# Performance work log

Measured on AMD Instinct MI355X. Metric: run time of the kernel, lower is better.

Reference implementation:

```python
import jax, jax.numpy as jnp
import numpy as np

D_MODEL = 1024


def bitlinear(x, weight):
    # ternary quantization with straight-through estimator; forward value is w_q*scale
    scale = jnp.clip(jnp.mean(jnp.abs(weight), axis=1, keepdims=True), 1e-5, None)
    w_q = jnp.clip(jnp.round(weight / scale), -1.0, 1.0)
    w = weight + jax.lax.stop_gradient(w_q * scale - weight)
    return x @ w.T


def rmsnorm(x, w, eps=1e-6):
    return x * jax.lax.rsqrt(jnp.mean(x * x, axis=-1, keepdims=True) + eps) * w


def setup_inputs() -> dict:
    key = jax.random.key(0)
    ks = jax.random.split(key, 6)
    D = D_MODEL
    std = np.sqrt(2.0 / D)  # kaiming_normal fan_out
    return {
        "x": jax.random.normal(ks[0], (4, 4096, D), dtype=jnp.float32),
        "Wr": jax.random.normal(ks[1], (D, D), dtype=jnp.float32) * std,
        "Wk": jax.random.normal(ks[2], (D, D), dtype=jnp.float32) * std,
        "Wv": jax.random.normal(ks[3], (D, D), dtype=jnp.float32) * std,
        "Wo": jax.random.normal(ks[4], (D, D), dtype=jnp.float32) * std,
        "decay": jnp.ones((D,), dtype=jnp.float32) * 0.99,
        "ln_w": jnp.ones((D,), dtype=jnp.float32),
    }


def reference(x, Wr, Wk, Wv, Wo, decay, ln_w):
    B, T, D = x.shape
    r = jax.nn.sigmoid(bitlinear(x, Wr))
    k = bitlinear(x, Wk)
    v = bitlinear(x, Wv)
    dec = jax.nn.sigmoid(decay)                              # [D]
    kv = k * v                                               # [B,T,D]
    positions = jnp.arange(T, dtype=x.dtype)                 # [T]
    log_decay = jnp.log(jnp.clip(dec, 1e-7, None))           # [D]
    scale = jnp.exp(positions[:, None] * log_decay[None, :])  # [T,D]
    scaled = kv / jnp.clip(scale, 1e-10, None)[None]         # [B,T,D]
    cum = jnp.cumsum(scaled, axis=1)                         # [B,T,D]
    state = cum * scale[None]                                # [B,T,D]
    return bitlinear(rmsnorm(r * state, ln_w), Wo)
```

## Files before the change

### kernel.cpp

```cpp
#include <hip/hip_runtime.h>

typedef unsigned short u16;
typedef __attribute__((ext_vector_type(8))) short bf16x8;
typedef __attribute__((ext_vector_type(4))) float f32x4;
typedef __attribute__((ext_vector_type(4))) unsigned short u16x4;

#define DM 1024

__device__ __forceinline__ float bf2f(u16 u){
  union { unsigned int i; float f; } v; v.i = ((unsigned int)u)<<16; return v.f;
}
__device__ __forceinline__ u16 f2bf(float f){
  unsigned int x = __float_as_uint(f);
  return (u16)((x + 0x7FFFu + ((x>>16)&1u)) >> 16);
}

__global__ __launch_bounds__(256)
void quantize_w(const float* __restrict__ W0, const float* __restrict__ W1,
                const float* __restrict__ W2, const float* __restrict__ W3,
                u16* __restrict__ wq, float* __restrict__ wsc)
{
  const int gr   = blockIdx.x*4 + (threadIdx.x>>6);
  const int lane = threadIdx.x & 63;
  const float* W; int row;
  if (gr < 1024)      { W = W0; row = gr; }
  else if (gr < 3072) { row = (gr-1024)>>1; W = (gr&1) ? W2 : W1; }
  else                { W = W3; row = gr-3072; }
  const float* wr = W + (size_t)row*DM;
  float4 v[4]; float s = 0.f;
  #pragma unroll
  for (int c=0;c<4;c++){
    v[c] = *(const float4*)&wr[c*256 + lane*4];
    s += fabsf(v[c].x)+fabsf(v[c].y)+fabsf(v[c].z)+fabsf(v[c].w);
  }
  #pragma unroll
  for (int off=32; off; off>>=1) s += __shfl_down(s, off);
  s = __shfl(s, 0);
  const float scale = fmaxf(s*(1.f/1024.f), 1e-5f);
  if (lane==0) wsc[gr] = scale;
  u16* wo = wq + (size_t)gr*DM;
  #pragma unroll
  for (int c=0;c<4;c++){
    u16x4 q;
    q[0] = f2bf(fminf(fmaxf(rintf(v[c].x/scale),-1.f),1.f));
    q[1] = f2bf(fminf(fmaxf(rintf(v[c].y/scale),-1.f),1.f));
    q[2] = f2bf(fminf(fmaxf(rintf(v[c].z/scale),-1.f),1.f));
    q[3] = f2bf(fminf(fmaxf(rintf(v[c].w/scale),-1.f),1.f));
    *(u16x4*)&wo[c*256 + lane*4] = q;
  }
}

__global__ void cvt_x(const float* __restrict__ x, u16* __restrict__ xb){
  const int i = (blockIdx.x*256 + threadIdx.x)*4;
  float4 v = *(const float4*)&x[i];
  u16x4 o; o[0]=f2bf(v.x); o[1]=f2bf(v.y); o[2]=f2bf(v.z); o[3]=f2bf(v.w);
  *(u16x4*)&xb[i] = o;
}


#define SB0 __builtin_amdgcn_sched_barrier(0)
#define WL4  do{ asm volatile("s_waitcnt lgkmcnt(4)" ::: "memory"); SB0; }while(0)
#define WL12 do{ asm volatile("s_waitcnt lgkmcnt(12)" ::: "memory"); SB0; }while(0)
#define WL0  do{ asm volatile("s_waitcnt lgkmcnt(0)" ::: "memory"); SB0; }while(0)
#define VM4  do{ asm volatile("s_waitcnt vmcnt(4)" ::: "memory"); SB0; }while(0)
#define VM0  do{ asm volatile("s_waitcnt vmcnt(0)" ::: "memory"); SB0; }while(0)
#define BARR do{ SB0; __builtin_amdgcn_s_barrier(); SB0; }while(0)

#define STG(gB, off, T, Q, buf) \
  __builtin_amdgcn_global_load_lds( \
    (const __attribute__((address_space(1))) void*)((const char*)(gB) + (off) + (Q)*131072 + (size_t)(T)*128), \
    (__attribute__((address_space(3))) void*)((char*)(buf) + ldst + (Q)*8192), 16, 0, 0)

#define RD(base, off) (*(const bf16x8*)((const char*)(base) + (off)))

#define MFMA16(AF, B, MI) \
  __builtin_amdgcn_s_setprio(1); \
  _Pragma("unroll") \
  for (int ni=0; ni<4; ++ni){ \
    acc[MI][ni]   = __builtin_amdgcn_mfma_f32_16x16x32_bf16(AF[0], B[ni],   acc[MI][ni],   0,0,0); \
    acc[MI][ni]   = __builtin_amdgcn_mfma_f32_16x16x32_bf16(AF[1], B[4+ni], acc[MI][ni],   0,0,0); \
    acc[MI+1][ni] = __builtin_amdgcn_mfma_f32_16x16x32_bf16(AF[2], B[ni],   acc[MI+1][ni], 0,0,0); \
    acc[MI+1][ni] = __builtin_amdgcn_mfma_f32_16x16x32_bf16(AF[3], B[4+ni], acc[MI+1][ni], 0,0,0); \
  } \
  __builtin_amdgcn_s_setprio(0)

#define TILE(T, C, BCUR, BNXT) { \
  const char* la  = (const char*)sA[C]; \
  const char* lnA = (const char*)sA[(C)^1]; \
  const char* lnB = (const char*)sB[(C)^1]; \
   \
  ay[0]=RD(la, arow+2*2048+koff0); ay[1]=RD(la, arow+2*2048+koff1); \
  ay[2]=RD(la, arow+3*2048+koff0); ay[3]=RD(la, arow+3*2048+koff1); \
  if ((T)+1<nt){ STG(Ag, aoff, (T)+1, 0, sA[(C)^1]); STG(Ag, aoff, (T)+1, 1, sA[(C)^1]); \
                 STG(Ag, aoff, (T)+1, 2, sA[(C)^1]); STG(Ag, aoff, (T)+1, 3, sA[(C)^1]); } \
  WL4; MFMA16(ax, BCUR, 0); BARR; \
   \
  ax[0]=RD(la, arow+4*2048+koff0); ax[1]=RD(la, arow+4*2048+koff1); \
  ax[2]=RD(la, arow+5*2048+koff0); ax[3]=RD(la, arow+5*2048+koff1); \
  if ((T)+2<nt){ STG(Bg, boff, (T)+2, 0, sB[C]); STG(Bg, boff, (T)+2, 1, sB[C]); } \
  WL4; MFMA16(ay, BCUR, 2); BARR; \
   \
  ay[0]=RD(la, arow+6*2048+koff0); ay[1]=RD(la, arow+6*2048+koff1); \
  ay[2]=RD(la, arow+7*2048+koff0); ay[3]=RD(la, arow+7*2048+koff1); \
  if ((T)+2<nt){ STG(Bg, boff, (T)+2, 2, sB[C]); STG(Bg, boff, (T)+2, 3, sB[C]); } \
  WL4; MFMA16(ax, BCUR, 4); SB0; \
  if ((T)==nt-2) { VM0; } else if ((T)<nt-2) { VM4; } \
  BARR; \
   \
  if ((T)<nt-1){ \
    BNXT[0]=RD(lnB, brow+0*2048+koff0); BNXT[1]=RD(lnB, brow+1*2048+koff0); \
    BNXT[2]=RD(lnB, brow+2*2048+koff0); BNXT[3]=RD(lnB, brow+3*2048+koff0); \
    BNXT[4]=RD(lnB, brow+0*2048+koff1); BNXT[5]=RD(lnB, brow+1*2048+koff1); \
    BNXT[6]=RD(lnB, brow+2*2048+koff1); BNXT[7]=RD(lnB, brow+3*2048+koff1); \
    ax[0]=RD(lnA, arow+0*2048+koff0); ax[1]=RD(lnA, arow+0*2048+koff1); \
    ax[2]=RD(lnA, arow+1*2048+koff0); ax[3]=RD(lnA, arow+1*2048+koff1); \
    WL12; \
  } else { WL0; } \
  MFMA16(ay, BCUR, 6); BARR; \
}

template<int MODE>
__global__ __launch_bounds__(512, 2)
void gemm_p(const u16* __restrict__ Ag, const u16* __restrict__ Bg,
            const float* __restrict__ bscale,
            u16* __restrict__ o_r, u16* __restrict__ o_kv,
            float* __restrict__ o_f)
{
  __shared__ u16 sA[2][256*64];
  __shared__ u16 sB[2][256*64];
  const int tid = threadIdx.x, wave = tid>>6, lane = tid&63;
  const int lr = lane&15, lg = lane>>4;
  const int wm = wave>>2, wn = wave&3;
  const int bm0 = blockIdx.x*256, bn0 = blockIdx.y*256;
  constexpr int nt = 16;

  const int r8   = lane>>3;
  const int scol = ((lane&7)<<4) ^ (r8<<4);
  const size_t aoff = (size_t)(bm0 + wave*8 + r8)*2048 + scol;
  const size_t boff = (size_t)(bn0 + wave*8 + r8)*2048 + scol;
  const int ldst = wave*1024;
  const int S = (lr&7)<<4;
  const int koff0 = (0  + (lg<<4)) ^ S;
  const int koff1 = (64 + (lg<<4)) ^ S;
  const int arow = (wm*128 + lr)*128;
  const int brow = (wn*64  + lr)*128;

  f32x4 acc[8][4];
  #pragma unroll
  for (int i=0;i<8;i++)
    #pragma unroll
    for (int j=0;j<4;j++) acc[i][j] = (f32x4){0.f,0.f,0.f,0.f};

  bf16x8 bc[8], bn2[8], ax[4], ay[4];

  #pragma unroll
  for (int q=0;q<4;q++){ STG(Ag, aoff, 0, q, sA[0]); STG(Bg, boff, 0, q, sB[0]); }
  #pragma unroll
  for (int q=0;q<4;q++){ STG(Bg, boff, 1, q, sB[1]); }
  VM4;
  BARR;
  {
    const char* la0 = (const char*)sA[0];
    const char* lb0 = (const char*)sB[0];
    bc[0]=RD(lb0, brow+0*2048+koff0); bc[1]=RD(lb0, brow+1*2048+koff0);
    bc[2]=RD(lb0, brow+2*2048+koff0); bc[3]=RD(lb0, brow+3*2048+koff0);
    bc[4]=RD(lb0, brow+0*2048+koff1); bc[5]=RD(lb0, brow+1*2048+koff1);
    bc[6]=RD(lb0, brow+2*2048+koff1); bc[7]=RD(lb0, brow+3*2048+koff1);
    ax[0]=RD(la0, arow+0*2048+koff0); ax[1]=RD(la0, arow+0*2048+koff1);
    ax[2]=RD(la0, arow+1*2048+koff0); ax[3]=RD(la0, arow+1*2048+koff1);
  }
  for (int tp=0; tp<nt; tp+=2){
    TILE(tp,   0, bc, bn2)
    TILE(tp+1, 1, bn2, bc)
  }

  #pragma unroll
  for (int mi=0; mi<8; ++mi){
    #pragma unroll
    for (int ni=0; ni<4; ++ni){
      const int col = bn0 + wn*64 + ni*16 + lr;
      const float sc = bscale[col];
      const int rowb = bm0 + wm*128 + mi*16 + lg*4;
      const f32x4 a = acc[mi][ni];
      if (MODE==0){
        if (bn0 < 1024){
          #pragma unroll
          for (int r2=0;r2<4;r2++){
            const float val = a[r2]*sc;
            o_r[(size_t)(rowb+r2)*DM + col] = f2bf(1.f/(1.f+expf(-val)));
          }
        } else {
          const int dv = (col - 1024) >> 1;
          #pragma unroll
          for (int r2=0;r2<4;r2++){
            const float val = a[r2]*sc;
            const float pr  = val * __shfl_xor(val, 1);
            if (!(lr & 1))
              o_kv[(size_t)(rowb+r2)*DM + dv] = f2bf(pr);
          }
        }
      } else {
        #pragma unroll
        for (int r2=0;r2<4;r2++)
          o_f[(size_t)(rowb+r2)*DM + col] = a[r2]*sc;
      }
    }
  }
}

__global__ __launch_bounds__(256)
void kv_phase1(const u16* __restrict__ kv, const float* __restrict__ decay,
               float* __restrict__ part)
{
  const int c = blockIdx.x & 127, b = blockIdx.x >> 7;
  const int d0 = threadIdx.x*4;
  float ld[4]; f32x4 sum = {0.f,0.f,0.f,0.f};
  #pragma unroll
  for (int j=0;j<4;j++){
    const float dec = 1.f/(1.f+expf(-decay[d0+j]));
    ld[j] = logf(fmaxf(dec, 1e-7f));
  }
  for (int t=c*32; t<c*32+32; ++t){
    const size_t base = ((size_t)(b*4096 + t))*DM + d0;
    const u16x4 p4 = *(const u16x4*)&kv[base];
    const float tf = (float)t;
    #pragma unroll
    for (int j=0;j<4;j++){
      const float e = expf(tf*ld[j]);
      sum[j] += bf2f(p4[j]) / fmaxf(e, 1e-10f);
    }
  }
  *(f32x4*)&part[((size_t)(b*128+c))*DM + d0] = sum;
}

__global__ void chunk_prefix(float* __restrict__ part){
  const int g = blockIdx.x*256 + threadIdx.x;
  const int b = g >> 8, d0 = (g & 255)*4;
  f32x4 run = {0.f,0.f,0.f,0.f};
  for (int c8=0; c8<128; c8+=8){
    f32x4 v[8];
    #pragma unroll
    for (int i=0;i<8;i++)
      v[i] = *(const f32x4*)&part[((size_t)(b*128+c8+i))*DM + d0];
    #pragma unroll
    for (int i=0;i<8;i++){
      const f32x4 tmp = v[i];
      *(f32x4*)&part[((size_t)(b*128+c8+i))*DM + d0] = run;
      run += tmp;
    }
  }
}

__global__ __launch_bounds__(256)
void scan_norm(const u16* __restrict__ kv, const u16* __restrict__ rbuf,
               const float* __restrict__ part, const float* __restrict__ decay,
               const float* __restrict__ lnw, u16* __restrict__ yn)
{
  const int c = blockIdx.x & 127, b = blockIdx.x >> 7;
  const int tid = threadIdx.x, lane = tid&63, wave = tid>>6;
  const int d0 = tid*4;
  __shared__ float red[2][4];
  f32x4 run = *(const f32x4*)&part[((size_t)(b*128+c))*DM + d0];
  float ld[4], lw[4];
  #pragma unroll
  for (int j=0;j<4;j++){
    const float dec = 1.f/(1.f+expf(-decay[d0+j]));
    ld[j] = logf(fmaxf(dec, 1e-7f));
    lw[j] = lnw[d0+j];
  }
  for (int t=c*32; t<c*32+32; ++t){
    const size_t base = ((size_t)(b*4096+t))*DM + d0;
    const u16x4 p4 = *(const u16x4*)&kv[base];
    const u16x4 r4 = *(const u16x4*)&rbuf[base];
    const float tf = (float)t;
    float y[4]; float ss = 0.f;
    #pragma unroll
    for (int j=0;j<4;j++){
      const float e = expf(tf*ld[j]);
      run[j] += bf2f(p4[j]) / fmaxf(e, 1e-10f);
      const float st = run[j]*e;
      y[j] = bf2f(r4[j])*st;
      ss += y[j]*y[j];
    }
    #pragma unroll
    for (int off=32; off; off>>=1) ss += __shfl_down(ss, off);
    if (lane==0) red[t&1][wave] = ss;
    __builtin_amdgcn_s_barrier();
    const float tot = (red[t&1][0]+red[t&1][1])+(red[t&1][2]+red[t&1][3]);
    const float rs = 1.f/sqrtf(tot*(1.f/1024.f) + 1e-6f);
    u16x4 o;
    #pragma unroll
    for (int j=0;j<4;j++) o[j] = f2bf(y[j]*rs*lw[j]);
    *(u16x4*)&yn[base] = o;
  }
}

extern "C" void kernel_launch(void* const* d_in, const int* in_sizes, int n_in,
                              void* d_out, int out_size, void* d_ws, size_t ws_size,
                              hipStream_t stream)
{
  (void)in_sizes; (void)n_in; (void)out_size; (void)ws_size;
  const float* x    = (const float*)d_in[0];
  const float* Wr   = (const float*)d_in[1];
  const float* Wk   = (const float*)d_in[2];
  const float* Wv   = (const float*)d_in[3];
  const float* Wo   = (const float*)d_in[4];
  const float* dec  = (const float*)d_in[5];
  const float* lnw  = (const float*)d_in[6];

  char* ws = (char*)d_ws;
  u16*   wq     = (u16*)(ws + 0);
  float* wsc    = (float*)(ws + 8388608);
  u16*   rbuf   = (u16*)(ws + 8404992);
  u16*   kvbuf  = (u16*)(ws + 41959424);
  float* part   = (float*)(ws + 75513856);
  u16*   xb     = (u16*)(ws + 77611008);
  u16*   yn     = (u16*)(ws + 111165440);

  quantize_w<<<1024, 256, 0, stream>>>(Wr, Wk, Wv, Wo, wq, wsc);
  cvt_x<<<16384, 256, 0, stream>>>(x, xb);
  gemm_p<0><<<dim3(64,12), 512, 0, stream>>>(xb, wq, wsc, rbuf, kvbuf, nullptr);
  kv_phase1<<<512, 256, 0, stream>>>(kvbuf, dec, part);
  chunk_prefix<<<4, 256, 0, stream>>>(part);
  scan_norm<<<512, 256, 0, stream>>>(kvbuf, rbuf, part, dec, lnw, yn);
  gemm_p<1><<<dim3(64,4), 512, 0, stream>>>(yn, wq + 3*1024*1024, wsc + 3072,
                                            nullptr, nullptr, (float*)d_out);
}
```

Measured before the change: 244.0 us.

## Replace pipelined 256x256 GEMM with simple single-buffered 128x128 tile kernel

Swaps the hand-scheduled, double-buffered 256x256-tile GEMM (512 threads, explicit waitcnt and sched barriers) for a plain 128x128-tile kernel with 256 threads, a single LDS buffer and __syncthreads around each K step. The aim is higher occupancy (4 blocks per CU) and more blocks in the grid, relying on wave interleaving instead of software pipelining to hide load latency. In exchange, global-to-LDS loads no longer overlap with MFMA work inside a block, and each output element's A and B tiles are reread more often from global memory.

```diff
diff --git a/kernel.cpp b/kernel.cpp
--- a/kernel.cpp
+++ b/kernel.cpp
@@ -58,80 +58,21 @@
 }
 
 
-#define SB0 __builtin_amdgcn_sched_barrier(0)
-#define WL4  do{ asm volatile("s_waitcnt lgkmcnt(4)" ::: "memory"); SB0; }while(0)
-#define WL12 do{ asm volatile("s_waitcnt lgkmcnt(12)" ::: "memory"); SB0; }while(0)
-#define WL0  do{ asm volatile("s_waitcnt lgkmcnt(0)" ::: "memory"); SB0; }while(0)
-#define VM4  do{ asm volatile("s_waitcnt vmcnt(4)" ::: "memory"); SB0; }while(0)
-#define VM0  do{ asm volatile("s_waitcnt vmcnt(0)" ::: "memory"); SB0; }while(0)
-#define BARR do{ SB0; __builtin_amdgcn_s_barrier(); SB0; }while(0)
-
-#define STG(gB, off, T, Q, buf) \
-  __builtin_amdgcn_global_load_lds( \
-    (const __attribute__((address_space(1))) void*)((const char*)(gB) + (off) + (Q)*131072 + (size_t)(T)*128), \
-    (__attribute__((address_space(3))) void*)((char*)(buf) + ldst + (Q)*8192), 16, 0, 0)
-
 #define RD(base, off) (*(const bf16x8*)((const char*)(base) + (off)))
 
-#define MFMA16(AF, B, MI) \
-  __builtin_amdgcn_s_setprio(1); \
-  _Pragma("unroll") \
-  for (int ni=0; ni<4; ++ni){ \
-    acc[MI][ni]   = __builtin_amdgcn_mfma_f32_16x16x32_bf16(AF[0], B[ni],   acc[MI][ni],   0,0,0); \
-    acc[MI][ni]   = __builtin_amdgcn_mfma_f32_16x16x32_bf16(AF[1], B[4+ni], acc[MI][ni],   0,0,0); \
-    acc[MI+1][ni] = __builtin_amdgcn_mfma_f32_16x16x32_bf16(AF[2], B[ni],   acc[MI+1][ni], 0,0,0); \
-    acc[MI+1][ni] = __builtin_amdgcn_mfma_f32_16x16x32_bf16(AF[3], B[4+ni], acc[MI+1][ni], 0,0,0); \
-  } \
-  __builtin_amdgcn_s_setprio(0)
-
-#define TILE(T, C, BCUR, BNXT) { \
-  const char* la  = (const char*)sA[C]; \
-  const char* lnA = (const char*)sA[(C)^1]; \
-  const char* lnB = (const char*)sB[(C)^1]; \
-   \
-  ay[0]=RD(la, arow+2*2048+koff0); ay[1]=RD(la, arow+2*2048+koff1); \
-  ay[2]=RD(la, arow+3*2048+koff0); ay[3]=RD(la, arow+3*2048+koff1); \
-  if ((T)+1<nt){ STG(Ag, aoff, (T)+1, 0, sA[(C)^1]); STG(Ag, aoff, (T)+1, 1, sA[(C)^1]); \
-                 STG(Ag, aoff, (T)+1, 2, sA[(C)^1]); STG(Ag, aoff, (T)+1, 3, sA[(C)^1]); } \
-  WL4; MFMA16(ax, BCUR, 0); BARR; \
-   \
-  ax[0]=RD(la, arow+4*2048+koff0); ax[1]=RD(la, arow+4*2048+koff1); \
-  ax[2]=RD(la, arow+5*2048+koff0); ax[3]=RD(la, arow+5*2048+koff1); \
-  if ((T)+2<nt){ STG(Bg, boff, (T)+2, 0, sB[C]); STG(Bg, boff, (T)+2, 1, sB[C]); } \
-  WL4; MFMA16(ay, BCUR, 2); BARR; \
-   \
-  ay[0]=RD(la, arow+6*2048+koff0); ay[1]=RD(la, arow+6*2048+koff1); \
-  ay[2]=RD(la, arow+7*2048+koff0); ay[3]=RD(la, arow+7*2048+koff1); \
-  if ((T)+2<nt){ STG(Bg, boff, (T)+2, 2, sB[C]); STG(Bg, boff, (T)+2, 3, sB[C]); } \
-  WL4; MFMA16(ax, BCUR, 4); SB0; \
-  if ((T)==nt-2) { VM0; } else if ((T)<nt-2) { VM4; } \
-  BARR; \
-   \
-  if ((T)<nt-1){ \
-    BNXT[0]=RD(lnB, brow+0*2048+koff0); BNXT[1]=RD(lnB, brow+1*2048+koff0); \
-    BNXT[2]=RD(lnB, brow+2*2048+koff0); BNXT[3]=RD(lnB, brow+3*2048+koff0); \
-    BNXT[4]=RD(lnB, brow+0*2048+koff1); BNXT[5]=RD(lnB, brow+1*2048+koff1); \
-    BNXT[6]=RD(lnB, brow+2*2048+koff1); BNXT[7]=RD(lnB, brow+3*2048+koff1); \
-    ax[0]=RD(lnA, arow+0*2048+koff0); ax[1]=RD(lnA, arow+0*2048+koff1); \
-    ax[2]=RD(lnA, arow+1*2048+koff0); ax[3]=RD(lnA, arow+1*2048+koff1); \
-    WL12; \
-  } else { WL0; } \
-  MFMA16(ay, BCUR, 6); BARR; \
-}
-
 template<int MODE>
-__global__ __launch_bounds__(512, 2)
-void gemm_p(const u16* __restrict__ Ag, const u16* __restrict__ Bg,
+__global__ __launch_bounds__(256, 4)
+void gemm_s(const u16* __restrict__ Ag, const u16* __restrict__ Bq,
             const float* __restrict__ bscale,
             u16* __restrict__ o_r, u16* __restrict__ o_kv,
             float* __restrict__ o_f)
 {
-  __shared__ u16 sA[2][256*64];
-  __shared__ u16 sB[2][256*64];
+  __shared__ u16 sA[128*64];
+  __shared__ u16 sB[128*64];
   const int tid = threadIdx.x, wave = tid>>6, lane = tid&63;
   const int lr = lane&15, lg = lane>>4;
-  const int wm = wave>>2, wn = wave&3;
-  const int bm0 = blockIdx.x*256, bn0 = blockIdx.y*256;
+  const int wm = wave>>1, wn = wave&1;
+  const int bm0 = blockIdx.x*128, bn0 = blockIdx.y*128;
   constexpr int nt = 16;
 
   const int r8   = lane>>3;
@@ -139,48 +80,61 @@
   const size_t aoff = (size_t)(bm0 + wave*8 + r8)*2048 + scol;
   const size_t boff = (size_t)(bn0 + wave*8 + r8)*2048 + scol;
   const int ldst = wave*1024;
+
   const int S = (lr&7)<<4;
-  const int koff0 = (0  + (lg<<4)) ^ S;
+  const int koff0 = ((lg<<4)     ) ^ S;
   const int koff1 = (64 + (lg<<4)) ^ S;
-  const int arow = (wm*128 + lr)*128;
-  const int brow = (wn*64  + lr)*128;
-
-  f32x4 acc[8][4];
-  #pragma unroll
-  for (int i=0;i<8;i++)
+  const int arow = (wm*64 + lr)*128;
+  const int brow = (wn*64 + lr)*128;
+
+  f32x4 acc[4][4];
+  #pragma unroll
+  for (int i=0;i<4;i++)
     #pragma unroll
     for (int j=0;j<4;j++) acc[i][j] = (f32x4){0.f,0.f,0.f,0.f};
 
-  bf16x8 bc[8], bn2[8], ax[4], ay[4];
-
-  #pragma unroll
-  for (int q=0;q<4;q++){ STG(Ag, aoff, 0, q, sA[0]); STG(Bg, boff, 0, q, sB[0]); }
-  #pragma unroll
-  for (int q=0;q<4;q++){ STG(Bg, boff, 1, q, sB[1]); }
-  VM4;
-  BARR;
-  {
-    const char* la0 = (const char*)sA[0];
-    const char* lb0 = (const char*)sB[0];
-    bc[0]=RD(lb0, brow+0*2048+koff0); bc[1]=RD(lb0, brow+1*2048+koff0);
-    bc[2]=RD(lb0, brow+2*2048+koff0); bc[3]=RD(lb0, brow+3*2048+koff0);
-    bc[4]=RD(lb0, brow+0*2048+koff1); bc[5]=RD(lb0, brow+1*2048+koff1);
-    bc[6]=RD(lb0, brow+2*2048+koff1); bc[7]=RD(lb0, brow+3*2048+koff1);
-    ax[0]=RD(la0, arow+0*2048+koff0); ax[1]=RD(la0, arow+0*2048+koff1);
-    ax[2]=RD(la0, arow+1*2048+koff0); ax[3]=RD(la0, arow+1*2048+koff1);
-  }
-  for (int tp=0; tp<nt; tp+=2){
-    TILE(tp,   0, bc, bn2)
-    TILE(tp+1, 1, bn2, bc)
-  }
-
-  #pragma unroll
-  for (int mi=0; mi<8; ++mi){
+  for (int t=0; t<nt; ++t){
+    #pragma unroll
+    for (int q=0;q<4;q++){
+      __builtin_amdgcn_global_load_lds(
+        (const __attribute__((address_space(1))) void*)((const char*)Ag + aoff + q*65536 + (size_t)t*128),
+        (__attribute__((address_space(3))) void*)((char*)sA + ldst + q*4096), 16, 0, 0);
+      __builtin_amdgcn_global_load_lds(
+        (const __attribute__((address_space(1))) void*)((const char*)Bq + boff + q*65536 + (size_t)t*128),
+        (__attribute__((address_space(3))) void*)((char*)sB + ldst + q*4096), 16, 0, 0);
+    }
+    __syncthreads();
+    {
+      bf16x8 a[4], b[4];
+      #pragma unroll
+      for (int m=0;m<4;m++) a[m] = RD(sA, arow + m*2048 + koff0);
+      #pragma unroll
+      for (int n=0;n<4;n++) b[n] = RD(sB, brow + n*2048 + koff0);
+      #pragma unroll
+      for (int m=0;m<4;m++)
+        #pragma unroll
+        for (int n=0;n<4;n++)
+          acc[m][n] = __builtin_amdgcn_mfma_f32_16x16x32_bf16(a[m], b[n], acc[m][n], 0,0,0);
+      #pragma unroll
+      for (int m=0;m<4;m++) a[m] = RD(sA, arow + m*2048 + koff1);
+      #pragma unroll
+      for (int n=0;n<4;n++) b[n] = RD(sB, brow + n*2048 + koff1);
+      #pragma unroll
+      for (int m=0;m<4;m++)
+        #pragma unroll
+        for (int n=0;n<4;n++)
+          acc[m][n] = __builtin_amdgcn_mfma_f32_16x16x32_bf16(a[m], b[n], acc[m][n], 0,0,0);
+    }
+    __syncthreads();
+  }
+
+  #pragma unroll
+  for (int mi=0; mi<4; ++mi){
     #pragma unroll
     for (int ni=0; ni<4; ++ni){
       const int col = bn0 + wn*64 + ni*16 + lr;
       const float sc = bscale[col];
-      const int rowb = bm0 + wm*128 + mi*16 + lg*4;
+      const int rowb = bm0 + wm*64 + mi*16 + lg*4;
       const f32x4 a = acc[mi][ni];
       if (MODE==0){
         if (bn0 < 1024){
@@ -319,10 +273,10 @@
 
   quantize_w<<<1024, 256, 0, stream>>>(Wr, Wk, Wv, Wo, wq, wsc);
   cvt_x<<<16384, 256, 0, stream>>>(x, xb);
-  gemm_p<0><<<dim3(64,12), 512, 0, stream>>>(xb, wq, wsc, rbuf, kvbuf, nullptr);
+  gemm_s<0><<<dim3(128,24), 256, 0, stream>>>(xb, wq, wsc, rbuf, kvbuf, nullptr);
   kv_phase1<<<512, 256, 0, stream>>>(kvbuf, dec, part);
   chunk_prefix<<<4, 256, 0, stream>>>(part);
   scan_norm<<<512, 256, 0, stream>>>(kvbuf, rbuf, part, dec, lnw, yn);
-  gemm_p<1><<<dim3(64,4), 512, 0, stream>>>(yn, wq + 3*1024*1024, wsc + 3072,
-                                            nullptr, nullptr, (float*)d_out);
-}
+  gemm_s<1><<<dim3(128,8), 256, 0, stream>>>(yn, wq + 3*1024*1024, wsc + 3072,
+                                             nullptr, nullptr, (float*)d_out);
+}
```

Measured after the change: 242.2 us. No clear change (-0.7%).
